# Optimization experiments

Measured on AMD Instinct MI355X. Metric: run time of the kernel, lower is better.

Reference implementation:

```python
import jax, jax.numpy as jnp
import numpy as np

EMBED_DIM = 1024
NUM_HEADS = 16
HEAD_DIM = EMBED_DIM // NUM_HEADS
LN_EPS = 1e-5


def setup_inputs() -> dict:
    key = jax.random.key(0)
    ks = jax.random.split(key, 13)
    b, n_q, k_len, E = 4, 2048, 2048, EMBED_DIM
    s = 1.0 / np.sqrt(E)
    inp = {
        "Q_input": jax.random.normal(ks[0], (b, n_q, E), jnp.float32),
        "K_input": jax.random.normal(ks[1], (b, k_len, E), jnp.float32),
        "V_input": jax.random.normal(ks[2], (b, k_len, E), jnp.float32),
        "Wq": jax.random.normal(ks[3], (E, E), jnp.float32) * s,
        "bq": jnp.zeros((E,), jnp.float32),
        "Wk": jax.random.normal(ks[4], (E, E), jnp.float32) * s,
        "bk": jnp.zeros((E,), jnp.float32),
        "Wv": jax.random.normal(ks[5], (E, E), jnp.float32) * s,
        "bv": jnp.zeros((E,), jnp.float32),
        "Wo": jax.random.normal(ks[6], (E, E), jnp.float32) * s,
        "bo": jnp.zeros((E,), jnp.float32),
        "gamma": jnp.ones((E,), jnp.float32),
        "beta": jnp.zeros((E,), jnp.float32),
    }
    return inp


def _layer_norm(x, gamma, beta):
    mu = jnp.mean(x, axis=-1, keepdims=True)
    var = jnp.mean(jnp.square(x - mu), axis=-1, keepdims=True)
    return (x - mu) * jax.lax.rsqrt(var + LN_EPS) * gamma + beta


def reference(Q_input, K_input, V_input, Wq, bq, Wk, bk, Wv, bv, Wo, bo, gamma, beta):
    b, n_q, E = Q_input.shape
    k_len = K_input.shape[1]
    H, D = NUM_HEADS, HEAD_DIM
    # projections (Linear: x @ W^T + b; here W stored as [E_in, E_out])
    Q = (Q_input @ Wq + bq).reshape(b, n_q, H, D).transpose(0, 2, 1, 3)   # [b,H,n_q,D]
    K = (K_input @ Wk + bk).reshape(b, k_len, H, D).transpose(0, 2, 1, 3)  # [b,H,k,D]
    V = (V_input @ Wv + bv).reshape(b, k_len, H, D).transpose(0, 2, 1, 3)
    scores = jnp.einsum('bhqd,bhkd->bhqk', Q, K) / jnp.sqrt(jnp.float32(D))
    attn = jax.nn.softmax(scores, axis=-1)
    ctx = jnp.einsum('bhqk,bhkd->bhqd', attn, V)           # [b,H,n_q,D]
    ctx = ctx.transpose(0, 2, 1, 3).reshape(b, n_q, E)
    out = ctx @ Wo + bo                                    # dropout = identity (eval)
    return _layer_norm(Q_input + out, gamma, beta)
```

## Files before the change

kernel.cpp:

```cpp
#include <hip/hip_runtime.h>

typedef __attribute__((ext_vector_type(8))) short s8v;
typedef __attribute__((ext_vector_type(4))) short s4v;
typedef __attribute__((ext_vector_type(4))) float f4v;

#define MFMA16(a, b, c) __builtin_amdgcn_mfma_f32_16x16x32_bf16((a), (b), (c), 0, 0, 0)
#define AS1 __attribute__((address_space(1)))
#define AS3 __attribute__((address_space(3)))

__device__ __forceinline__ short f2bf(float f) {
  union { float f; unsigned u; } v; v.f = f;
  unsigned r = v.u + 0x7FFFu + ((v.u >> 16) & 1u);
  return (short)(r >> 16);
}
__device__ __forceinline__ unsigned fbits(float f) {
  union { float f; unsigned u; } v; v.f = f; return v.u;
}
__device__ __forceinline__ unsigned pack2(float hi, float lo) {
  return __builtin_amdgcn_perm(fbits(hi), fbits(lo), 0x07060302u);
}
__device__ __forceinline__ void gld16(const void* g, void* l) {
  __builtin_amdgcn_global_load_lds((const AS1 unsigned*)g, (AS3 unsigned*)l, 16, 0, 0);
}

__global__ __launch_bounds__(256) void castbf(const float* __restrict__ in0,
                                              const float* __restrict__ in1,
                                              short* __restrict__ out) {
  const float* in = blockIdx.y ? in1 : in0;
  out += (size_t)blockIdx.y * 8388608;
  int g = blockIdx.x * 256 + threadIdx.x;
  for (int i = 0; i < 4; ++i) {
    int idx = g + i * 524288;
    float4 v = ((const float4*)in)[idx];
    s4v o = { f2bf(v.x), f2bf(v.y), f2bf(v.z), f2bf(v.w) };
    ((s4v*)out)[idx] = o;
  }
}

__global__ __launch_bounds__(256) void wtrans4(const float* __restrict__ W0,
                                               const float* __restrict__ W1,
                                               const float* __restrict__ W2,
                                               const float* __restrict__ W3,
                                               short* __restrict__ Wt) {
  const float* W = blockIdx.z == 0 ? W0 : blockIdx.z == 1 ? W1 : blockIdx.z == 2 ? W2 : W3;
  Wt += (size_t)blockIdx.z * 1048576;
  __shared__ float tile[64][65];
  const int r0 = blockIdx.y * 64, c0 = blockIdx.x * 64;
  const int t = threadIdx.x;
  for (int i = 0; i < 4; ++i) {
    int lin = t + i * 256;
    int row = lin >> 4, c4 = (lin & 15) << 2;
    float4 v = *(const float4*)(W + (size_t)(r0 + row) * 1024 + c0 + c4);
    tile[row][c4 + 0] = v.x; tile[row][c4 + 1] = v.y;
    tile[row][c4 + 2] = v.z; tile[row][c4 + 3] = v.w;
  }
  __syncthreads();
  for (int i = 0; i < 4; ++i) {
    int lin = t + i * 256;
    int nl = lin >> 4, k4 = (lin & 15) << 2;
    s4v sv = { f2bf(tile[k4 + 0][nl]), f2bf(tile[k4 + 1][nl]),
               f2bf(tile[k4 + 2][nl]), f2bf(tile[k4 + 3][nl]) };
    *(s4v*)&Wt[(size_t)(c0 + nl) * 1024 + r0 + k4] = sv;
  }
}

template <int OUT>
__global__ __launch_bounds__(256) void gemm_bt(
    const short* __restrict__ A, const short* __restrict__ Bt,
    const float* __restrict__ bias0, const float* __restrict__ bias1,
    float s0, float s1,
    short* __restrict__ outb, float* __restrict__ outf) {
  __shared__ __align__(16) short As[128 * 32];
  __shared__ __align__(16) short Bs[128 * 32];
  const int z = blockIdx.z;
  A += (size_t)z * 8388608;
  Bt += (size_t)z * 1048576;
  outb += (size_t)z * 8388608;
  const float* bias = z ? bias1 : bias0;
  const float scale = z ? s1 : s0;

  const int tid = threadIdx.x;
  const int lane = tid & 63, w = tid >> 6;
  const int quad = lane >> 4, l16 = lane & 15;
  const int wm = (w >> 1) * 64, wn = (w & 1) * 64;
  const int mBase = blockIdx.x * 128, nBase = blockIdx.y * 128;
  f4v acc[4][4] = {};

  const int id0 = tid, id1 = tid + 256;
  const int r0 = id0 >> 2, c0 = (id0 & 3) << 3;
  const int r1 = id1 >> 2, c1 = (id1 & 3) << 3;
  const short* Ag0 = A + (size_t)(mBase + r0) * 1024 + c0;
  const short* Ag1 = A + (size_t)(mBase + r1) * 1024 + c1;
  const short* Bg0 = Bt + (size_t)(nBase + r0) * 1024 + c0;
  const short* Bg1 = Bt + (size_t)(nBase + r1) * 1024 + c1;

  for (int kt = 0; kt < 32; ++kt) {
    __syncthreads();
    gld16(Ag0 + kt * 32, &As[id0 * 8]);
    gld16(Ag1 + kt * 32, &As[id1 * 8]);
    gld16(Bg0 + kt * 32, &Bs[id0 * 8]);
    gld16(Bg1 + kt * 32, &Bs[id1 * 8]);
    __syncthreads();
    s8v a[4], b[4];
    for (int mt = 0; mt < 4; ++mt) a[mt] = *(const s8v*)&As[(wm + mt * 16 + l16) * 32 + quad * 8];
    for (int nt = 0; nt < 4; ++nt) b[nt] = *(const s8v*)&Bs[(wn + nt * 16 + l16) * 32 + quad * 8];
    for (int mt = 0; mt < 4; ++mt)
      for (int nt = 0; nt < 4; ++nt)
        acc[mt][nt] = MFMA16(a[mt], b[nt], acc[mt][nt]);
  }

  if constexpr (OUT == 2) {
    __shared__ short Ts[128 * 136];
    for (int nt = 0; nt < 4; ++nt) {
      int colg = nBase + wn + nt * 16 + l16;
      float bs = bias[colg];
      for (int mt = 0; mt < 4; ++mt)
        for (int r = 0; r < 4; ++r)
          Ts[(wn + nt * 16 + l16) * 136 + wm + mt * 16 + quad * 4 + r] =
              f2bf(acc[mt][nt][r] + bs);
    }
    __syncthreads();
    const int bI = mBase >> 11, tok0 = mBase & 2047;
    for (int it = 0; it < 8; ++it) {
      int dloc = (tid >> 4) + it * 16;
      int tok8 = (tid & 15) << 3;
      s8v v = *(const s8v*)&Ts[dloc * 136 + tok8];
      int colg = nBase + dloc;
      int h = colg >> 6, d = colg & 63;
      *(s8v*)&outb[(((size_t)bI * 16 + h) * 64 + d) * 2048 + tok0 + tok8] = v;
    }
  } else {
    for (int nt = 0; nt < 4; ++nt) {
      int col = nBase + wn + nt * 16 + l16;
      float bs = bias[col];
      for (int mt = 0; mt < 4; ++mt) {
        for (int r = 0; r < 4; ++r) {
          int row = mBase + wm + mt * 16 + quad * 4 + r;
          float val = (acc[mt][nt][r] + bs) * scale;
          if constexpr (OUT == 0) {
            int b = row >> 11, token = row & 2047, h = col >> 6, d = col & 63;
            outb[(((size_t)b * 16 + h) * 2048 + token) * 64 + d] = f2bf(val);
          } else {
            outf[(size_t)row * 1024 + col] = val;
          }
        }
      }
    }
  }
}

__global__ __launch_bounds__(256, 2) void attn_kernel(
    const short* __restrict__ Qp, const short* __restrict__ Kp,
    const short* __restrict__ Vpt, short* __restrict__ Ctx) {
  __shared__ __align__(16) short Ks[64][72];
  __shared__ __align__(16) short Vt[64][72];

  const int tid = threadIdx.x, w = tid >> 6, lane = tid & 63;
  const int quad = lane >> 4, l16 = lane & 15;
  const int qt = blockIdx.x, bh = blockIdx.y;
  const short* Qb = Qp + (size_t)bh * 2048 * 64;
  const short* Kb = Kp + (size_t)bh * 2048 * 64;
  const short* Vb = Vpt + (size_t)bh * 64 * 2048;
  const int qbase = qt * 256 + w * 64;

  s8v qf[4][2];
#pragma unroll
  for (int mt = 0; mt < 4; ++mt)
#pragma unroll
    for (int h = 0; h < 2; ++h)
      qf[mt][h] = *(const s8v*)(Qb + (size_t)(qbase + mt * 16 + l16) * 64 + h * 32 + quad * 8);

  const s8v vone = {16256, 16256, 16256, 16256, 16256, 16256, 16256, 16256};
  f4v Oa[4][4] = {};
  f4v La[4] = {};

  for (int kv = 0; kv < 32; ++kv) {
    const int kv0 = kv * 64;
    __syncthreads();
#pragma unroll
    for (int i = 0; i < 2; ++i) {
      int id = tid + i * 256;
      int g = id >> 3, c8 = (id & 7) << 3;
      int p = (g & 32) | (((g >> 2) & 1) << 4) | (((g >> 3) & 3) << 2) | (g & 3);
      *(s8v*)&Ks[p][c8] = *(const s8v*)(Kb + (size_t)(kv0 + g) * 64 + c8);
      *(s8v*)&Vt[g][c8] = *(const s8v*)(Vb + (size_t)g * 2048 + kv0 + c8);
    }
    __syncthreads();

    s8v kf[4][2], vf[4][2];
#pragma unroll
    for (int T = 0; T < 4; ++T) {
      kf[T][0] = *(const s8v*)&Ks[T * 16 + l16][quad * 8];
      kf[T][1] = *(const s8v*)&Ks[T * 16 + l16][32 + quad * 8];
      vf[T][0] = *(const s8v*)&Vt[T * 16 + l16][quad * 8];
      vf[T][1] = *(const s8v*)&Vt[T * 16 + l16][32 + quad * 8];
    }

#pragma unroll
    for (int mt = 0; mt < 4; ++mt) {
      f4v s[4] = {};
#pragma unroll
      for (int T = 0; T < 4; ++T) {
        s[T] = MFMA16(kf[T][0], qf[mt][0], s[T]);
        s[T] = MFMA16(kf[T][1], qf[mt][1], s[T]);
      }
#pragma unroll
      for (int T = 0; T < 4; ++T)
#pragma unroll
        for (int r = 0; r < 4; ++r)
          s[T][r] = __builtin_amdgcn_exp2f(s[T][r]);
      s8v pf[2];
#pragma unroll
      for (int cp = 0; cp < 2; ++cp) {
        union { s8v v; unsigned u[4]; } pk;
        pk.u[0] = pack2(s[2 * cp][1], s[2 * cp][0]);
        pk.u[1] = pack2(s[2 * cp][3], s[2 * cp][2]);
        pk.u[2] = pack2(s[2 * cp + 1][1], s[2 * cp + 1][0]);
        pk.u[3] = pack2(s[2 * cp + 1][3], s[2 * cp + 1][2]);
        pf[cp] = pk.v;
      }
      La[mt] = MFMA16(pf[0], vone, La[mt]);
      La[mt] = MFMA16(pf[1], vone, La[mt]);
#pragma unroll
      for (int nt = 0; nt < 4; ++nt) {
        Oa[mt][nt] = MFMA16(pf[0], vf[nt][0], Oa[mt][nt]);
        Oa[mt][nt] = MFMA16(pf[1], vf[nt][1], Oa[mt][nt]);
      }
    }
  }

  const int b = bh >> 4, h = bh & 15;
#pragma unroll
  for (int mt = 0; mt < 4; ++mt)
#pragma unroll
    for (int r = 0; r < 4; ++r) {
      float inv = 1.f / La[mt][r];
      int q = qbase + mt * 16 + quad * 4 + r;
#pragma unroll
      for (int nt = 0; nt < 4; ++nt) {
        int d = nt * 16 + l16;
        Ctx[((size_t)b * 2048 + q) * 1024 + h * 64 + d] = f2bf(Oa[mt][nt][r] * inv);
      }
    }
}

__global__ __launch_bounds__(256) void ln_kernel(
    const float* __restrict__ resid, const float* __restrict__ attn,
    const float* __restrict__ gamma, const float* __restrict__ beta,
    float* __restrict__ out) {
  const int row = blockIdx.x, t = threadIdx.x;
  const float4 rv = *(const float4*)(resid + (size_t)row * 1024 + t * 4);
  const float4 av = *(const float4*)(attn + (size_t)row * 1024 + t * 4);
  float x0 = rv.x + av.x, x1 = rv.y + av.y, x2 = rv.z + av.z, x3 = rv.w + av.w;
  float s = x0 + x1 + x2 + x3;
  float ss = x0 * x0 + x1 * x1 + x2 * x2 + x3 * x3;
  for (int off = 32; off > 0; off >>= 1) {
    s += __shfl_down(s, off, 64);
    ss += __shfl_down(ss, off, 64);
  }
  __shared__ float red[8];
  const int wid = t >> 6, lane = t & 63;
  if (lane == 0) { red[wid] = s; red[4 + wid] = ss; }
  __syncthreads();
  float S = red[0] + red[1] + red[2] + red[3];
  float SS = red[4] + red[5] + red[6] + red[7];
  float mu = S * (1.f / 1024.f);
  float var = SS * (1.f / 1024.f) - mu * mu;
  float rstd = rsqrtf(var + 1e-5f);
  const float4 g = *(const float4*)(gamma + t * 4);
  const float4 bb = *(const float4*)(beta + t * 4);
  float4 o;
  o.x = (x0 - mu) * rstd * g.x + bb.x;
  o.y = (x1 - mu) * rstd * g.y + bb.y;
  o.z = (x2 - mu) * rstd * g.z + bb.z;
  o.w = (x3 - mu) * rstd * g.w + bb.w;
  *(float4*)(out + (size_t)row * 1024 + t * 4) = o;
}

extern "C" void kernel_launch(void* const* d_in, const int* in_sizes, int n_in,
                              void* d_out, int out_size, void* d_ws, size_t ws_size,
                              hipStream_t stream) {
  const float* Qin = (const float*)d_in[0];
  const float* Kin = (const float*)d_in[1];
  const float* Vin = (const float*)d_in[2];
  const float* Wq = (const float*)d_in[3];
  const float* bq = (const float*)d_in[4];
  const float* Wk = (const float*)d_in[5];
  const float* bk = (const float*)d_in[6];
  const float* Wv = (const float*)d_in[7];
  const float* bv = (const float*)d_in[8];
  const float* Wo = (const float*)d_in[9];
  const float* bo = (const float*)d_in[10];
  const float* gamma = (const float*)d_in[11];
  const float* beta = (const float*)d_in[12];
  float* out = (float*)d_out;

  char* ws = (char*)d_ws;
  const size_t MB = 1024 * 1024;
  short* Ab  = (short*)(ws);
  short* Qp  = (short*)(ws + 32 * MB);
  short* Kp  = (short*)(ws + 48 * MB);
  short* Vpt = (short*)(ws + 64 * MB);
  short* Wt  = (short*)(ws + 80 * MB);
  short* Ctx = (short*)(ws);
  float* AOut = (float*)(ws + 16 * MB);

  wtrans4<<<dim3(16, 16, 4), 256, 0, stream>>>(Wq, Wk, Wv, Wo, Wt);

  const float qscale = 0.125f * 1.44269504f;

  castbf<<<dim3(2048, 2), 256, 0, stream>>>(Qin, Kin, Ab);
  gemm_bt<0><<<dim3(64, 8, 2), 256, 0, stream>>>(Ab, Wt, bq, bk, qscale, 1.f, Qp, nullptr);

  castbf<<<dim3(2048, 1), 256, 0, stream>>>(Vin, nullptr, Ab);
  gemm_bt<2><<<dim3(64, 8, 1), 256, 0, stream>>>(Ab, Wt + 2 * 1048576, bv, nullptr, 1.f, 0.f, Vpt, nullptr);

  attn_kernel<<<dim3(8, 64), 256, 0, stream>>>(Qp, Kp, Vpt, Ctx);

  gemm_bt<1><<<dim3(64, 8, 1), 256, 0, stream>>>(Ctx, Wt + 3 * 1048576, bo, nullptr, 1.f, 0.f, nullptr, AOut);

  ln_kernel<<<8192, 256, 0, stream>>>(Qin, AOut, gamma, beta, out);
}
```

Baseline: 363.7 us.

## Fuse fp32-to-bf16 cast into QKV GEMM, batch QKV launch, bf16 output projection

```diff
diff --git a/kernel.cpp b/kernel.cpp
--- a/kernel.cpp
+++ b/kernel.cpp
@@ -13,6 +13,10 @@
   unsigned r = v.u + 0x7FFFu + ((v.u >> 16) & 1u);
   return (short)(r >> 16);
 }
+__device__ __forceinline__ float bf2f(short s) {
+  union { unsigned u; float f; } v; v.u = ((unsigned)(unsigned short)s) << 16;
+  return v.f;
+}
 __device__ __forceinline__ unsigned fbits(float f) {
   union { float f; unsigned u; } v; v.f = f; return v.u;
 }
@@ -21,20 +25,6 @@
 }
 __device__ __forceinline__ void gld16(const void* g, void* l) {
   __builtin_amdgcn_global_load_lds((const AS1 unsigned*)g, (AS3 unsigned*)l, 16, 0, 0);
-}
-
-__global__ __launch_bounds__(256) void castbf(const float* __restrict__ in0,
-                                              const float* __restrict__ in1,
-                                              short* __restrict__ out) {
-  const float* in = blockIdx.y ? in1 : in0;
-  out += (size_t)blockIdx.y * 8388608;
-  int g = blockIdx.x * 256 + threadIdx.x;
-  for (int i = 0; i < 4; ++i) {
-    int idx = g + i * 524288;
-    float4 v = ((const float4*)in)[idx];
-    s4v o = { f2bf(v.x), f2bf(v.y), f2bf(v.z), f2bf(v.w) };
-    ((s4v*)out)[idx] = o;
-  }
 }
 
 __global__ __launch_bounds__(256) void wtrans4(const float* __restrict__ W0,
@@ -64,20 +54,26 @@
   }
 }
 
-template <int OUT>
+template <int CAST, int EPI>
 __global__ __launch_bounds__(256) void gemm_bt(
-    const short* __restrict__ A, const short* __restrict__ Bt,
-    const float* __restrict__ bias0, const float* __restrict__ bias1,
-    float s0, float s1,
-    short* __restrict__ outb, float* __restrict__ outf) {
+    const float* __restrict__ Af0, const float* __restrict__ Af1,
+    const float* __restrict__ Af2, const short* __restrict__ Ab,
+    const short* __restrict__ Bt,
+    const float* __restrict__ b0, const float* __restrict__ b1,
+    const float* __restrict__ b2, float s0,
+    short* __restrict__ outb) {
   __shared__ __align__(16) short As[128 * 32];
   __shared__ __align__(16) short Bs[128 * 32];
+  __shared__ __align__(16) char Ebuf[18432];
+  short (*Ta)[136] = (short(*)[136])Ebuf;
+  short (*Tv)[72]  = (short(*)[72])Ebuf;
+
   const int z = blockIdx.z;
-  A += (size_t)z * 8388608;
+  const float* Af = (CAST && z == 1) ? Af1 : (CAST && z == 2) ? Af2 : Af0;
   Bt += (size_t)z * 1048576;
   outb += (size_t)z * 8388608;
-  const float* bias = z ? bias1 : bias0;
-  const float scale = z ? s1 : s0;
+  const float* bias = z == 0 ? b0 : z == 1 ? b1 : b2;
+  const float scale = z == 0 ? s0 : 1.f;
 
   const int tid = threadIdx.x;
   const int lane = tid & 63, w = tid >> 6;
@@ -87,19 +83,36 @@
   f4v acc[4][4] = {};
 
   const int id0 = tid, id1 = tid + 256;
-  const int r0 = id0 >> 2, c0 = (id0 & 3) << 3;
-  const int r1 = id1 >> 2, c1 = (id1 & 3) << 3;
-  const short* Ag0 = A + (size_t)(mBase + r0) * 1024 + c0;
-  const short* Ag1 = A + (size_t)(mBase + r1) * 1024 + c1;
-  const short* Bg0 = Bt + (size_t)(nBase + r0) * 1024 + c0;
-  const short* Bg1 = Bt + (size_t)(nBase + r1) * 1024 + c1;
+  const short* Bg0 = Bt + (size_t)((id0 >> 2) + nBase) * 1024 + ((id0 & 3) << 3);
+  const short* Bg1 = Bt + (size_t)((id1 >> 2) + nBase) * 1024 + ((id1 & 3) << 3);
+  const float* Ap[4];
+  const short* Ag0 = nullptr; const short* Ag1 = nullptr;
+  short* Al[4];
+  if constexpr (CAST) {
+    for (int i = 0; i < 4; ++i) {
+      int id = tid + i * 256;
+      Ap[i] = Af + (size_t)(mBase + (id >> 3)) * 1024 + ((id & 7) << 2);
+      Al[i] = &As[(id >> 3) * 32 + ((id & 7) << 2)];
+    }
+  } else {
+    Ag0 = Ab + (size_t)((id0 >> 2) + mBase) * 1024 + ((id0 & 3) << 3);
+    Ag1 = Ab + (size_t)((id1 >> 2) + mBase) * 1024 + ((id1 & 3) << 3);
+  }
 
   for (int kt = 0; kt < 32; ++kt) {
     __syncthreads();
-    gld16(Ag0 + kt * 32, &As[id0 * 8]);
-    gld16(Ag1 + kt * 32, &As[id1 * 8]);
     gld16(Bg0 + kt * 32, &Bs[id0 * 8]);
     gld16(Bg1 + kt * 32, &Bs[id1 * 8]);
+    if constexpr (CAST) {
+      for (int i = 0; i < 4; ++i) {
+        float4 v = *(const float4*)(Ap[i] + kt * 32);
+        s4v sv = { f2bf(v.x), f2bf(v.y), f2bf(v.z), f2bf(v.w) };
+        *(s4v*)Al[i] = sv;
+      }
+    } else {
+      gld16(Ag0 + kt * 32, &As[id0 * 8]);
+      gld16(Ag1 + kt * 32, &As[id1 * 8]);
+    }
     __syncthreads();
     s8v a[4], b[4];
     for (int mt = 0; mt < 4; ++mt) a[mt] = *(const s8v*)&As[(wm + mt * 16 + l16) * 32 + quad * 8];
@@ -109,40 +122,41 @@
         acc[mt][nt] = MFMA16(a[mt], b[nt], acc[mt][nt]);
   }
 
-  if constexpr (OUT == 2) {
-    __shared__ short Ts[128 * 136];
-    for (int nt = 0; nt < 4; ++nt) {
-      int colg = nBase + wn + nt * 16 + l16;
-      float bs = bias[colg];
-      for (int mt = 0; mt < 4; ++mt)
-        for (int r = 0; r < 4; ++r)
-          Ts[(wn + nt * 16 + l16) * 136 + wm + mt * 16 + quad * 4 + r] =
-              f2bf(acc[mt][nt][r] + bs);
-    }
-    __syncthreads();
-    const int bI = mBase >> 11, tok0 = mBase & 2047;
-    for (int it = 0; it < 8; ++it) {
-      int dloc = (tid >> 4) + it * 16;
-      int tok8 = (tid & 15) << 3;
-      s8v v = *(const s8v*)&Ts[dloc * 136 + tok8];
-      int colg = nBase + dloc;
-      int h = colg >> 6, d = colg & 63;
-      *(s8v*)&outb[(((size_t)bI * 16 + h) * 64 + d) * 2048 + tok0 + tok8] = v;
-    }
-  } else {
-    for (int nt = 0; nt < 4; ++nt) {
-      int col = nBase + wn + nt * 16 + l16;
-      float bs = bias[col];
-      for (int mt = 0; mt < 4; ++mt) {
-        for (int r = 0; r < 4; ++r) {
-          int row = mBase + wm + mt * 16 + quad * 4 + r;
-          float val = (acc[mt][nt][r] + bs) * scale;
-          if constexpr (OUT == 0) {
-            int b = row >> 11, token = row & 2047, h = col >> 6, d = col & 63;
-            outb[(((size_t)b * 16 + h) * 2048 + token) * 64 + d] = f2bf(val);
-          } else {
-            outf[(size_t)row * 1024 + col] = val;
+  const int bI = mBase >> 11, tok0 = mBase & 2047;
+  const bool vpath = (EPI == 0) && (z == 2);
+  for (int p = 0; p < 2; ++p) {
+    __syncthreads();
+    if ((w >> 1) == p) {
+      for (int nt = 0; nt < 4; ++nt) {
+        int featl = wn + nt * 16 + l16;
+        float bs = bias[nBase + featl];
+        for (int mt = 0; mt < 4; ++mt)
+          for (int r = 0; r < 4; ++r) {
+            short val = f2bf((acc[mt][nt][r] + bs) * scale);
+            if (vpath) Tv[featl][mt * 16 + quad * 4 + r] = val;
+            else       Ta[mt * 16 + quad * 4 + r][featl] = val;
           }
+      }
+    }
+    __syncthreads();
+    if (vpath) {
+      for (int it = 0; it < 4; ++it) {
+        int id = tid + it * 256;
+        int f = id >> 3, t8 = (id & 7) << 3;
+        s8v v = *(const s8v*)&Tv[f][t8];
+        int gf = nBase + f, h = gf >> 6, d = gf & 63;
+        *(s8v*)&outb[(((size_t)bI * 16 + h) * 64 + d) * 2048 + tok0 + p * 64 + t8] = v;
+      }
+    } else {
+      for (int it = 0; it < 4; ++it) {
+        int id = tid + it * 256;
+        int tok = id >> 4, f8 = (id & 15) << 3;
+        s8v v = *(const s8v*)&Ta[tok][f8];
+        if constexpr (EPI == 1) {
+          *(s8v*)&outb[(size_t)(mBase + p * 64 + tok) * 1024 + nBase + f8] = v;
+        } else {
+          int gf = nBase + f8, h = gf >> 6, d = gf & 63;
+          *(s8v*)&outb[(((size_t)bI * 16 + h) * 2048 + tok0 + p * 64 + tok) * 64 + d] = v;
         }
       }
     }
@@ -245,13 +259,14 @@
 }
 
 __global__ __launch_bounds__(256) void ln_kernel(
-    const float* __restrict__ resid, const float* __restrict__ attn,
+    const float* __restrict__ resid, const short* __restrict__ attnb,
     const float* __restrict__ gamma, const float* __restrict__ beta,
     float* __restrict__ out) {
   const int row = blockIdx.x, t = threadIdx.x;
   const float4 rv = *(const float4*)(resid + (size_t)row * 1024 + t * 4);
-  const float4 av = *(const float4*)(attn + (size_t)row * 1024 + t * 4);
-  float x0 = rv.x + av.x, x1 = rv.y + av.y, x2 = rv.z + av.z, x3 = rv.w + av.w;
+  const s4v av = *(const s4v*)(attnb + (size_t)row * 1024 + t * 4);
+  float x0 = rv.x + bf2f(av[0]), x1 = rv.y + bf2f(av[1]);
+  float x2 = rv.z + bf2f(av[2]), x3 = rv.w + bf2f(av[3]);
   float s = x0 + x1 + x2 + x3;
   float ss = x0 * x0 + x1 * x1 + x2 * x2 + x3 * x3;
   for (int off = 32; off > 0; off >>= 1) {
@@ -297,27 +312,22 @@
 
   char* ws = (char*)d_ws;
   const size_t MB = 1024 * 1024;
-  short* Ab  = (short*)(ws);
-  short* Qp  = (short*)(ws + 32 * MB);
-  short* Kp  = (short*)(ws + 48 * MB);
-  short* Vpt = (short*)(ws + 64 * MB);
-  short* Wt  = (short*)(ws + 80 * MB);
-  short* Ctx = (short*)(ws);
-  float* AOut = (float*)(ws + 16 * MB);
+  short* Qp    = (short*)(ws);
+  short* Ctx   = (short*)(ws + 48 * MB);
+  short* AOutB = (short*)(ws + 64 * MB);
+  short* Wt    = (short*)(ws + 80 * MB);
 
   wtrans4<<<dim3(16, 16, 4), 256, 0, stream>>>(Wq, Wk, Wv, Wo, Wt);
 
   const float qscale = 0.125f * 1.44269504f;
 
-  castbf<<<dim3(2048, 2), 256, 0, stream>>>(Qin, Kin, Ab);
-  gemm_bt<0><<<dim3(64, 8, 2), 256, 0, stream>>>(Ab, Wt, bq, bk, qscale, 1.f, Qp, nullptr);
-
-  castbf<<<dim3(2048, 1), 256, 0, stream>>>(Vin, nullptr, Ab);
-  gemm_bt<2><<<dim3(64, 8, 1), 256, 0, stream>>>(Ab, Wt + 2 * 1048576, bv, nullptr, 1.f, 0.f, Vpt, nullptr);
-
-  attn_kernel<<<dim3(8, 64), 256, 0, stream>>>(Qp, Kp, Vpt, Ctx);
-
-  gemm_bt<1><<<dim3(64, 8, 1), 256, 0, stream>>>(Ctx, Wt + 3 * 1048576, bo, nullptr, 1.f, 0.f, nullptr, AOut);
-
-  ln_kernel<<<8192, 256, 0, stream>>>(Qin, AOut, gamma, beta, out);
-}
+  gemm_bt<1, 0><<<dim3(64, 8, 3), 256, 0, stream>>>(
+      Qin, Kin, Vin, nullptr, Wt, bq, bk, bv, qscale, Qp);
+
+  attn_kernel<<<dim3(8, 64), 256, 0, stream>>>(Qp, Qp + 8388608, Qp + 16777216, Ctx);
+
+  gemm_bt<0, 1><<<dim3(64, 8, 1), 256, 0, stream>>>(
+      nullptr, nullptr, nullptr, Ctx, Wt + 3 * 1048576, bo, bo, bo, 1.f, AOutB);
+
+  ln_kernel<<<8192, 256, 0, stream>>>(Qin, AOutB, gamma, beta, out);
+}
```

Result: slower. 399.9 us (+10.0%).
